# Kernel optimization log

Measured on AMD Instinct MI355X. Metric: run time of the kernel, lower is better.

The kernel has to match this reference:

```python
import jax, jax.numpy as jnp
import numpy as np

DIM = 256
HEADS = 8
HEAD_DIM = DIM // HEADS
SCALE = HEAD_DIM ** -0.5
EPS_LN = 1e-5
EPS_NORM = 1e-12


def setup_inputs() -> dict:
    key = jax.random.key(0)
    ks = jax.random.split(key, 12)
    B, C, H, W = 8, DIM, 32, 32
    s = 0.02
    return {
        "x": jax.random.normal(ks[0], (B, C, H, W), jnp.float32),
        "dw_w": jax.random.normal(ks[1], (C, 1, 3, 3), jnp.float32) * s,
        "dw_b": jnp.zeros((C,), jnp.float32),
        "qkv_w": jax.random.normal(ks[2], (3 * C, C), jnp.float32) * s,
        "c1_w": jax.random.normal(ks[3], (C, C), jnp.float32) * s,
        "c1_b": jnp.zeros((C,), jnp.float32),
        "ln1_g": jnp.ones((C,), jnp.float32),
        "ln1_b": jnp.zeros((C,), jnp.float32),
        "c2_w": jax.random.normal(ks[4], (C, C), jnp.float32) * s,
        "c2_b": jnp.zeros((C,), jnp.float32),
        "ln2_g": jnp.ones((C,), jnp.float32),
        "ln2_b": jnp.zeros((C,), jnp.float32),
    }


def _l2norm(t):
    n = jnp.sqrt(jnp.sum(t * t, axis=-1, keepdims=True))
    return t / jnp.maximum(n, EPS_NORM)


def _layernorm_c(x_nchw, g, b):
    # LayerNorm over channel dim of an NCHW tensor (torch does permute->LN->permute)
    mu = jnp.mean(x_nchw, axis=1, keepdims=True)
    var = jnp.mean((x_nchw - mu) ** 2, axis=1, keepdims=True)
    xn = (x_nchw - mu) * jax.lax.rsqrt(var + EPS_LN)
    return xn * g[None, :, None, None] + b[None, :, None, None]


def _gelu(x):
    return jax.nn.gelu(x, approximate=False)


def reference(x, dw_w, dw_b, qkv_w, c1_w, c1_b, ln1_g, ln1_b, c2_w, c2_b, ln2_g, ln2_b):
    B, C, H, W = x.shape
    identity = x
    # depthwise 3x3 conv
    y = jax.lax.conv_general_dilated(
        x, dw_w, window_strides=(1, 1), padding="SAME",
        dimension_numbers=("NCHW", "OIHW", "NCHW"), feature_group_count=C)
    y = y + dw_b[None, :, None, None]
    # tokens [B, N, C]
    t = y.reshape(B, C, H * W).transpose(0, 2, 1)
    qkv = jnp.einsum("bnc,oc->bno", t, qkv_w)  # [B,N,3C]
    qkv = qkv.reshape(B, H * W, 3, HEADS, HEAD_DIM).transpose(2, 0, 3, 1, 4)
    q, k, v = qkv[0], qkv[1], qkv[2]  # [B,h,N,d]
    q = _l2norm(q)
    k = _l2norm(k)
    attn = jnp.einsum("bhnd,bhmd->bhnm", q, k) * SCALE
    attn = jax.nn.softmax(attn, axis=-1)
    o = jnp.einsum("bhnm,bhmd->bhnd", attn, v)  # [B,h,N,d]
    o = o.transpose(0, 2, 1, 3).reshape(B, H * W, C)
    y = o.transpose(0, 2, 1).reshape(B, C, H, W)
    # conv-MLP branch (1x1 convs as channel GEMMs)
    y = jnp.einsum("bchw,oc->bohw", y, c1_w) + c1_b[None, :, None, None]
    y = _gelu(_layernorm_c(y, ln1_g, ln1_b))
    y = jnp.einsum("bchw,oc->bohw", y, c2_w) + c2_b[None, :, None, None]
    y = _gelu(_layernorm_c(y, ln2_g, ln2_b))
    return identity + y
```

## Files before the change

### kernel.cpp

```cpp
#include <hip/hip_runtime.h>
#include <math.h>

#define DIMC 256
#define NTOK 1024
#define QKVN 768
#define HDIM 32

typedef __attribute__((ext_vector_type(8))) short bf16x8;
typedef __attribute__((ext_vector_type(4))) float f32x4;
typedef __attribute__((ext_vector_type(4))) unsigned short us4;

__device__ __forceinline__ unsigned short f2bf(float f) {
  unsigned u = __float_as_uint(f);
  u += 0x7FFF + ((u >> 16) & 1);
  return (unsigned short)(u >> 16);
}

__device__ __forceinline__ float gelu_f(float y) {
  return 0.5f * y * (1.f + erff(y * 0.70710678118654752f));
}

__global__ void dwconv_k(const float* __restrict__ x, const float* __restrict__ w,
                         const float* __restrict__ b, float* __restrict__ y) {
  int bc = blockIdx.x;
  int c = bc & (DIMC - 1);
  float wr[9];
#pragma unroll
  for (int i = 0; i < 9; i++) wr[i] = w[c * 9 + i];
  float bb = b[c];
  const float* xp = x + (size_t)bc * NTOK;
  float* yp = y + (size_t)bc * NTOK;
  for (int p = threadIdx.x; p < NTOK; p += 256) {
    int hh = p >> 5, ww = p & 31;
    float acc = bb;
#pragma unroll
    for (int dh = 0; dh < 3; dh++) {
      int h2 = hh + dh - 1;
      if ((unsigned)h2 < 32u) {
#pragma unroll
        for (int dw = 0; dw < 3; dw++) {
          int w2 = ww + dw - 1;
          if ((unsigned)w2 < 32u) acc += xp[h2 * 32 + w2] * wr[dh * 3 + dw];
        }
      }
    }
    yp[p] = acc;
  }
}

__global__ void cvt_w_k(const float* __restrict__ w0, const float* __restrict__ w1,
                        const float* __restrict__ w2, unsigned short* __restrict__ Wb) {
  int i = (blockIdx.x * 256 + threadIdx.x) * 4;
  const float* src;
  int off;
  if (i < 196608) { src = w0; off = i; }
  else if (i < 262144) { src = w1; off = i - 196608; }
  else { src = w2; off = i - 262144; }
  float4 v = *(const float4*)(src + off);
  us4 o = {f2bf(v.x), f2bf(v.y), f2bf(v.z), f2bf(v.w)};
  *(us4*)(Wb + i) = o;
}

__global__ void t2b_k(const float* __restrict__ y2, unsigned short* __restrict__ A0) {
  __shared__ float tile[32][33];
  int b = blockIdx.z, c0 = blockIdx.y << 5, s0 = blockIdx.x << 5;
  int t = threadIdx.x;
  int j = t & 31, i0 = t >> 5;
#pragma unroll
  for (int i = i0; i < 32; i += 8)
    tile[i][j] = y2[(size_t)(b * 256 + c0 + i) * 1024 + s0 + j];
  __syncthreads();
#pragma unroll
  for (int i2 = i0; i2 < 32; i2 += 8)
    A0[(size_t)(b * 1024 + s0 + i2) * 256 + c0 + j] = f2bf(tile[j][i2]);
}

template <bool BIAS>
__global__ __launch_bounds__(256) void mgemm_k(const unsigned short* __restrict__ A,
                                               const unsigned short* __restrict__ W,
                                               const float* __restrict__ bias,
                                               float* __restrict__ C, int N) {
  __shared__ __align__(16) unsigned short As[128 * 40];
  __shared__ __align__(16) unsigned short Bs[64 * 40];
  const int t = threadIdx.x;
  const int m0 = blockIdx.y * 128;
  const int n0 = blockIdx.x * 64;
  const int wid = t >> 6, lane = t & 63;
  const int lg = lane >> 4, lr = lane & 15;
  const int wm0 = (wid >> 1) * 64, wn0 = (wid & 1) * 32;

  f32x4 acc[4][2] = {};
  for (int k0 = 0; k0 < 256; k0 += 32) {
    __syncthreads();
    {
#pragma unroll
      for (int u = 0; u < 2; u++) {
        int f = t + u * 256;
        int r = f >> 2, c = f & 3;
        bf16x8 v = *(const bf16x8*)(A + (size_t)(m0 + r) * 256 + k0 + c * 8);
        *(bf16x8*)&As[r * 40 + c * 8] = v;
      }
      int o = t >> 2, c = t & 3;
      bf16x8 v = *(const bf16x8*)(W + (size_t)(n0 + o) * 256 + k0 + c * 8);
      *(bf16x8*)&Bs[o * 40 + c * 8] = v;
    }
    __syncthreads();
    bf16x8 af[4], bfr[2];
#pragma unroll
    for (int mt = 0; mt < 4; mt++)
      af[mt] = *(const bf16x8*)&As[(wm0 + mt * 16 + lr) * 40 + lg * 8];
#pragma unroll
    for (int nt = 0; nt < 2; nt++)
      bfr[nt] = *(const bf16x8*)&Bs[(wn0 + nt * 16 + lr) * 40 + lg * 8];
#pragma unroll
    for (int mt = 0; mt < 4; mt++)
#pragma unroll
      for (int nt = 0; nt < 2; nt++)
        acc[mt][nt] = __builtin_amdgcn_mfma_f32_16x16x32_bf16(af[mt], bfr[nt], acc[mt][nt], 0, 0, 0);
  }
  float bv[2];
#pragma unroll
  for (int nt = 0; nt < 2; nt++)
    bv[nt] = BIAS ? bias[n0 + wn0 + nt * 16 + lr] : 0.f;
#pragma unroll
  for (int mt = 0; mt < 4; mt++)
#pragma unroll
    for (int nt = 0; nt < 2; nt++)
#pragma unroll
      for (int r = 0; r < 4; r++) {
        int row = m0 + wm0 + mt * 16 + lg * 4 + r;
        int col = n0 + wn0 + nt * 16 + lr;
        C[(size_t)row * N + col] = acc[mt][nt][r] + bv[nt];
      }
}

__global__ void cvt_qkv_k(const float* __restrict__ qkv,
                          unsigned short* __restrict__ Qb,
                          unsigned short* __restrict__ Kb) {
  int n = blockIdx.x;
  int t = threadIdx.x;
  int b = n >> 10, nr = n & 1023;
  int sec = t >> 6, lane = t & 63;
  const float* p = qkv + (size_t)n * QKVN + sec * 256 + lane * 4;
  float4 v = *(const float4*)p;
  float s = v.x * v.x + v.y * v.y + v.z * v.z + v.w * v.w;
  s += __shfl_xor(s, 1, 64); s += __shfl_xor(s, 2, 64); s += __shfl_xor(s, 4, 64);
  float inv = 1.f / fmaxf(sqrtf(s), 1e-12f);
  if (sec == 0) inv *= 0.17677669529663687f;
  int h = lane >> 3, d4 = (lane & 7) << 2;
  unsigned short* dst = (sec == 0 ? Qb : Kb) + ((size_t)((b * 8 + h) * 1024 + nr)) * 32 + d4;
  us4 o = {f2bf(v.x * inv), f2bf(v.y * inv), f2bf(v.z * inv), f2bf(v.w * inv)};
  *(us4*)dst = o;
}

#define VPAD 66
__global__ __launch_bounds__(256) void vT_k(const float* __restrict__ qkv,
                                            unsigned short* __restrict__ Vt) {
  __shared__ unsigned short Vl[32 * VPAD];
  const int tt = blockIdx.x, bh = blockIdx.y;
  const int b = bh >> 3, h = bh & 7;
  const int n0 = tt * 64;
  const int t = threadIdx.x;
  {
    int nl = t >> 2, d8 = (t & 3) * 8;
    const float* p = qkv + (size_t)(b * 1024 + n0 + nl) * QKVN + 512 + h * 32 + d8;
    float4 a = *(const float4*)p;
    float4 c = *(const float4*)(p + 4);
    float vv[8] = {a.x, a.y, a.z, a.w, c.x, c.y, c.z, c.w};
#pragma unroll
    for (int i = 0; i < 8; i++) Vl[(d8 + i) * VPAD + nl] = f2bf(vv[i]);
  }
  __syncthreads();
  {
    int d = t >> 3, seg = t & 7;
    us4 lo = *(const us4*)&Vl[d * VPAD + seg * 8];
    us4 hi = *(const us4*)&Vl[d * VPAD + seg * 8 + 4];
    unsigned short* dst = Vt + ((size_t)(bh * 32 + d) << 10) + n0 + seg * 8;
    *(us4*)dst = lo;
    *(us4*)(dst + 4) = hi;
  }
}

#define PSTR 36

__global__ __launch_bounds__(64) void attn_mfma_k(const unsigned short* __restrict__ Qb,
                                                  const unsigned short* __restrict__ Kb,
                                                  const unsigned short* __restrict__ Vt,
                                                  unsigned short* __restrict__ obuf) {
  __shared__ __align__(16) unsigned short Pl[32 * PSTR];
  const int bh = blockIdx.y;
  const int q0 = blockIdx.x * 32;
  const int lane = threadIdx.x;
  const int lg = lane >> 4, lr = lane & 15;
  const size_t base = (size_t)bh * NTOK;
  const unsigned short* vb = Vt + ((size_t)bh * 32 << 10);

  bf16x8 qf[2];
#pragma unroll
  for (int qt = 0; qt < 2; qt++)
    qf[qt] = *(const bf16x8*)(Qb + (base + q0 + qt * 16 + lr) * 32 + lg * 8);

  f32x4 o[2][2] = {};
  float lpart[2][4] = {};

  for (int step = 0; step < 32; step++) {
    const int kv0 = step * 32;
    bf16x8 kf[2];
#pragma unroll
    for (int ct = 0; ct < 2; ct++)
      kf[ct] = *(const bf16x8*)(Kb + (base + kv0 + ct * 16 + lr) * 32 + lg * 8);
#pragma unroll
    for (int qt = 0; qt < 2; qt++) {
#pragma unroll
      for (int ct = 0; ct < 2; ct++) {
        f32x4 c = {};
        c = __builtin_amdgcn_mfma_f32_16x16x32_bf16(qf[qt], kf[ct], c, 0, 0, 0);
#pragma unroll
        for (int r = 0; r < 4; r++) {
          float p = __expf(c[r]);
          lpart[qt][r] += p;
          Pl[(qt * 16 + lg * 4 + r) * PSTR + ct * 16 + lr] = f2bf(p);
        }
      }
    }
#pragma unroll
    for (int qt = 0; qt < 2; qt++) {
      us4 plo = *(const us4*)&Pl[(qt * 16 + lr) * PSTR + lg * 8];
      us4 phi = *(const us4*)&Pl[(qt * 16 + lr) * PSTR + lg * 8 + 4];
      bf16x8 pf = {(short)plo[0], (short)plo[1], (short)plo[2], (short)plo[3],
                   (short)phi[0], (short)phi[1], (short)phi[2], (short)phi[3]};
#pragma unroll
      for (int dt = 0; dt < 2; dt++) {
        bf16x8 vf = *(const bf16x8*)(vb + ((size_t)(dt * 16 + lr) << 10) + kv0 + lg * 8);
        o[qt][dt] = __builtin_amdgcn_mfma_f32_16x16x32_bf16(pf, vf, o[qt][dt], 0, 0, 0);
      }
    }
  }
#pragma unroll
  for (int qt = 0; qt < 2; qt++) {
#pragma unroll
    for (int r = 0; r < 4; r++) {
      float l = lpart[qt][r];
      l += __shfl_xor(l, 1, 64); l += __shfl_xor(l, 2, 64);
      l += __shfl_xor(l, 4, 64); l += __shfl_xor(l, 8, 64);
      lpart[qt][r] = 1.f / l;
    }
  }
  const int b = bh >> 3, h = bh & 7;
#pragma unroll
  for (int qt = 0; qt < 2; qt++)
#pragma unroll
    for (int dt = 0; dt < 2; dt++)
#pragma unroll
      for (int r = 0; r < 4; r++) {
        int q = q0 + qt * 16 + lg * 4 + r;
        int c = h * 32 + dt * 16 + lr;
        obuf[((size_t)(b * NTOK + q)) * DIMC + c] = f2bf(o[qt][dt][r] * lpart[qt][r]);
      }
}

template <bool OBF>
__global__ void ln_gelu_k(const float* __restrict__ in, const float* __restrict__ g,
                          const float* __restrict__ bb, void* __restrict__ outv) {
  int t = threadIdx.x;
  int lane = t & 63;
  int r = blockIdx.x * 4 + (t >> 6);
  const float* p = in + ((size_t)r << 8) + (lane << 2);
  float4 v = *(const float4*)p;
  float s1 = v.x + v.y + v.z + v.w;
  float s2 = v.x * v.x + v.y * v.y + v.z * v.z + v.w * v.w;
#pragma unroll
  for (int m = 1; m < 64; m <<= 1) {
    s1 += __shfl_xor(s1, m, 64);
    s2 += __shfl_xor(s2, m, 64);
  }
  float mu = s1 * (1.f / 256.f);
  float var = s2 * (1.f / 256.f) - mu * mu;
  float rstd = rsqrtf(var + 1e-5f);
  float4 gv = *(const float4*)(g + (lane << 2));
  float4 bv = *(const float4*)(bb + (lane << 2));
  float4 ov;
  ov.x = gelu_f((v.x - mu) * rstd * gv.x + bv.x);
  ov.y = gelu_f((v.y - mu) * rstd * gv.y + bv.y);
  ov.z = gelu_f((v.z - mu) * rstd * gv.z + bv.z);
  ov.w = gelu_f((v.w - mu) * rstd * gv.w + bv.w);
  if (OBF) {
    us4 ob = {f2bf(ov.x), f2bf(ov.y), f2bf(ov.z), f2bf(ov.w)};
    *(us4*)((unsigned short*)outv + ((size_t)r << 8) + (lane << 2)) = ob;
  } else {
    *(float4*)((float*)outv + ((size_t)r << 8) + (lane << 2)) = ov;
  }
}

__global__ void trans_add_k(const float* __restrict__ m2, const float* __restrict__ x,
                            float* __restrict__ out) {
  __shared__ float tile[32][33];
  int b = blockIdx.z, c0 = blockIdx.y << 5, s0 = blockIdx.x << 5;
  int t = threadIdx.x;
  int j = t & 31, i0 = t >> 5;
#pragma unroll
  for (int i = i0; i < 32; i += 8)
    tile[i][j] = m2[(size_t)(b * 1024 + s0 + i) * 256 + c0 + j];
  __syncthreads();
#pragma unroll
  for (int i2 = i0; i2 < 32; i2 += 8) {
    size_t idx = ((size_t)(b * 256 + c0 + i2) << 10) + s0 + j;
    out[idx] = x[idx] + tile[j][i2];
  }
}

extern "C" void kernel_launch(void* const* d_in, const int* in_sizes, int n_in,
                              void* d_out, int out_size, void* d_ws, size_t ws_size,
                              hipStream_t stream) {
  const float* x     = (const float*)d_in[0];
  const float* dw_w  = (const float*)d_in[1];
  const float* dw_b  = (const float*)d_in[2];
  const float* qkv_w = (const float*)d_in[3];
  const float* c1_w  = (const float*)d_in[4];
  const float* c1_b  = (const float*)d_in[5];
  const float* ln1_g = (const float*)d_in[6];
  const float* ln1_b = (const float*)d_in[7];
  const float* c2_w  = (const float*)d_in[8];
  const float* c2_b  = (const float*)d_in[9];
  const float* ln2_g = (const float*)d_in[10];
  const float* ln2_b = (const float*)d_in[11];
  float* out = (float*)d_out;

  float* ws = (float*)d_ws;
  const size_t MF = (size_t)1 << 20;
  float* y2   = ws;
  unsigned short* A0 = (unsigned short*)(ws + 2 * MF);
  unsigned short* Wb = (unsigned short*)(ws + 3 * MF);
  float* qkv  = ws + 4 * MF;
  unsigned short* Qb = (unsigned short*)(ws + 10 * MF);
  unsigned short* Kb = (unsigned short*)(ws + 11 * MF);
  unsigned short* Vtb = (unsigned short*)(ws + 12 * MF);
  unsigned short* obuf = (unsigned short*)ws;
  unsigned short* m1 = (unsigned short*)(ws + 1 * MF);
  float* buf1 = ws + 4 * MF;
  float* buf2 = ws + 6 * MF;
  float* m2b  = ws + 8 * MF;
  (void)in_sizes; (void)n_in; (void)out_size; (void)ws_size;

  dwconv_k<<<2048, 256, 0, stream>>>(x, dw_w, dw_b, y2);
  cvt_w_k<<<320, 256, 0, stream>>>(qkv_w, c1_w, c2_w, Wb);
  t2b_k<<<dim3(32, 8, 8), 256, 0, stream>>>(y2, A0);
  mgemm_k<false><<<dim3(12, 64), 256, 0, stream>>>(A0, Wb, nullptr, qkv, 768);
  cvt_qkv_k<<<8192, 128, 0, stream>>>(qkv, Qb, Kb);
  vT_k<<<dim3(16, 64), 256, 0, stream>>>(qkv, Vtb);
  attn_mfma_k<<<dim3(32, 64), 64, 0, stream>>>(Qb, Kb, Vtb, obuf);
  mgemm_k<true><<<dim3(4, 64), 256, 0, stream>>>(obuf, Wb + 196608, c1_b, buf1, 256);
  ln_gelu_k<true><<<2048, 256, 0, stream>>>(buf1, ln1_g, ln1_b, m1);
  mgemm_k<true><<<dim3(4, 64), 256, 0, stream>>>(m1, Wb + 262144, c2_b, buf2, 256);
  ln_gelu_k<false><<<2048, 256, 0, stream>>>(buf2, ln2_g, ln2_b, m2b);
  trans_add_k<<<dim3(32, 8, 8), 256, 0, stream>>>(m2b, x, out);
}
```

Before: 178.3 us.

## Fuse dwconv with transpose/cast, QK-norm with V transpose, LN2 with residual transpose

Merges the depthwise conv, weight conversion and token-major bf16 transpose into one kernel, so the fp32 conv output no longer makes a round trip through global memory. The Q/K normalisation is folded into the V-transpose kernel, and the second LayerNorm+GELU is fused with the NCHW transpose and residual add through a shared-memory tile. Together these drop three launches and several intermediate buffers. In exchange, the fused LN/transpose kernel runs only 256 blocks with a large shared tile, and the conv kernel reloads halo rows for each block.

```diff
diff --git a/kernel.cpp b/kernel.cpp
--- a/kernel.cpp
+++ b/kernel.cpp
@@ -20,59 +20,64 @@
   return 0.5f * y * (1.f + erff(y * 0.70710678118654752f));
 }
 
-__global__ void dwconv_k(const float* __restrict__ x, const float* __restrict__ w,
-                         const float* __restrict__ b, float* __restrict__ y) {
-  int bc = blockIdx.x;
-  int c = bc & (DIMC - 1);
-  float wr[9];
-#pragma unroll
-  for (int i = 0; i < 9; i++) wr[i] = w[c * 9 + i];
-  float bb = b[c];
-  const float* xp = x + (size_t)bc * NTOK;
-  float* yp = y + (size_t)bc * NTOK;
-  for (int p = threadIdx.x; p < NTOK; p += 256) {
-    int hh = p >> 5, ww = p & 31;
-    float acc = bb;
+__global__ __launch_bounds__(256) void dwt_k(const float* __restrict__ x,
+                                             const float* __restrict__ w,
+                                             const float* __restrict__ b,
+                                             unsigned short* __restrict__ A0,
+                                             const float* __restrict__ w0,
+                                             const float* __restrict__ w1,
+                                             const float* __restrict__ w2,
+                                             unsigned short* __restrict__ Wb) {
+  int blk = blockIdx.x;
+  int t = threadIdx.x;
+  if (blk >= 2048) {
+    int i = ((blk - 2048) * 256 + t) * 4;
+    const float* src;
+    int off;
+    if (i < 196608) { src = w0; off = i; }
+    else if (i < 262144) { src = w1; off = i - 196608; }
+    else { src = w2; off = i - 262144; }
+    float4 v = *(const float4*)(src + off);
+    us4 o = {f2bf(v.x), f2bf(v.y), f2bf(v.z), f2bf(v.w)};
+    *(us4*)(Wb + i) = o;
+    return;
+  }
+  __shared__ float xs[32][3][33];
+  __shared__ float ws9[32][9];
+  __shared__ float bs[32];
+  const int b_ = blk >> 8, h = (blk >> 3) & 31, c0 = (blk & 7) << 5;
+  {
+    int cl = t >> 3, seg = (t & 7) << 2;
+    const float* xp = x + ((size_t)(b_ * 256 + c0 + cl) << 10);
 #pragma unroll
     for (int dh = 0; dh < 3; dh++) {
-      int h2 = hh + dh - 1;
-      if ((unsigned)h2 < 32u) {
-#pragma unroll
-        for (int dw = 0; dw < 3; dw++) {
-          int w2 = ww + dw - 1;
-          if ((unsigned)w2 < 32u) acc += xp[h2 * 32 + w2] * wr[dh * 3 + dw];
-        }
-      }
-    }
-    yp[p] = acc;
-  }
-}
-
-__global__ void cvt_w_k(const float* __restrict__ w0, const float* __restrict__ w1,
-                        const float* __restrict__ w2, unsigned short* __restrict__ Wb) {
-  int i = (blockIdx.x * 256 + threadIdx.x) * 4;
-  const float* src;
-  int off;
-  if (i < 196608) { src = w0; off = i; }
-  else if (i < 262144) { src = w1; off = i - 196608; }
-  else { src = w2; off = i - 262144; }
-  float4 v = *(const float4*)(src + off);
-  us4 o = {f2bf(v.x), f2bf(v.y), f2bf(v.z), f2bf(v.w)};
-  *(us4*)(Wb + i) = o;
-}
-
-__global__ void t2b_k(const float* __restrict__ y2, unsigned short* __restrict__ A0) {
-  __shared__ float tile[32][33];
-  int b = blockIdx.z, c0 = blockIdx.y << 5, s0 = blockIdx.x << 5;
-  int t = threadIdx.x;
-  int j = t & 31, i0 = t >> 5;
-#pragma unroll
-  for (int i = i0; i < 32; i += 8)
-    tile[i][j] = y2[(size_t)(b * 256 + c0 + i) * 1024 + s0 + j];
+      int h2 = h + dh - 1;
+      float4 v = {0.f, 0.f, 0.f, 0.f};
+      if ((unsigned)h2 < 32u) v = *(const float4*)(xp + h2 * 32 + seg);
+      xs[cl][dh][seg + 0] = v.x; xs[cl][dh][seg + 1] = v.y;
+      xs[cl][dh][seg + 2] = v.z; xs[cl][dh][seg + 3] = v.w;
+    }
+  }
+  for (int i = t; i < 288; i += 256) ws9[i / 9][i % 9] = w[(c0 + i / 9) * 9 + i % 9];
+  if (t < 32) bs[t] = b[c0 + t];
   __syncthreads();
-#pragma unroll
-  for (int i2 = i0; i2 < 32; i2 += 8)
-    A0[(size_t)(b * 1024 + s0 + i2) * 256 + c0 + j] = f2bf(tile[j][i2]);
+  const int wp = t >> 3, cq = (t & 7) << 2;
+  us4 o;
+#pragma unroll
+  for (int j = 0; j < 4; j++) {
+    int c = cq + j;
+    float acc = bs[c];
+#pragma unroll
+    for (int dh = 0; dh < 3; dh++) {
+#pragma unroll
+      for (int dw = 0; dw < 3; dw++) {
+        int w2 = wp + dw - 1;
+        if ((unsigned)w2 < 32u) acc += xs[c][dh][w2] * ws9[c][dh * 3 + dw];
+      }
+    }
+    o[j] = f2bf(acc);
+  }
+  *(us4*)(A0 + (((size_t)(b_ * 1024 + h * 32 + wp)) << 8) + c0 + cq) = o;
 }
 
 template <bool BIAS>
@@ -134,33 +139,39 @@
       }
 }
 
-__global__ void cvt_qkv_k(const float* __restrict__ qkv,
-                          unsigned short* __restrict__ Qb,
-                          unsigned short* __restrict__ Kb) {
-  int n = blockIdx.x;
-  int t = threadIdx.x;
-  int b = n >> 10, nr = n & 1023;
-  int sec = t >> 6, lane = t & 63;
-  const float* p = qkv + (size_t)n * QKVN + sec * 256 + lane * 4;
-  float4 v = *(const float4*)p;
-  float s = v.x * v.x + v.y * v.y + v.z * v.z + v.w * v.w;
-  s += __shfl_xor(s, 1, 64); s += __shfl_xor(s, 2, 64); s += __shfl_xor(s, 4, 64);
-  float inv = 1.f / fmaxf(sqrtf(s), 1e-12f);
-  if (sec == 0) inv *= 0.17677669529663687f;
-  int h = lane >> 3, d4 = (lane & 7) << 2;
-  unsigned short* dst = (sec == 0 ? Qb : Kb) + ((size_t)((b * 8 + h) * 1024 + nr)) * 32 + d4;
-  us4 o = {f2bf(v.x * inv), f2bf(v.y * inv), f2bf(v.z * inv), f2bf(v.w * inv)};
-  *(us4*)dst = o;
-}
-
 #define VPAD 66
-__global__ __launch_bounds__(256) void vT_k(const float* __restrict__ qkv,
-                                            unsigned short* __restrict__ Vt) {
+__global__ __launch_bounds__(256) void qkvprep_k(const float* __restrict__ qkv,
+                                                 unsigned short* __restrict__ Qb,
+                                                 unsigned short* __restrict__ Kb,
+                                                 unsigned short* __restrict__ Vt) {
   __shared__ unsigned short Vl[32 * VPAD];
   const int tt = blockIdx.x, bh = blockIdx.y;
   const int b = bh >> 3, h = bh & 7;
   const int n0 = tt * 64;
   const int t = threadIdx.x;
+  {
+    int pair = t >> 7, idx = t & 127;
+    int nl = idx >> 1, e0 = (idx & 1) << 4;
+    const float* p = qkv + (size_t)(b * 1024 + n0 + nl) * QKVN + pair * 256 + h * 32 + e0;
+    float4 v0 = *(const float4*)(p + 0);
+    float4 v1 = *(const float4*)(p + 4);
+    float4 v2 = *(const float4*)(p + 8);
+    float4 v3 = *(const float4*)(p + 12);
+    float s = v0.x * v0.x + v0.y * v0.y + v0.z * v0.z + v0.w * v0.w
+            + v1.x * v1.x + v1.y * v1.y + v1.z * v1.z + v1.w * v1.w
+            + v2.x * v2.x + v2.y * v2.y + v2.z * v2.z + v2.w * v2.w
+            + v3.x * v3.x + v3.y * v3.y + v3.z * v3.z + v3.w * v3.w;
+    s += __shfl_xor(s, 1, 64);
+    float inv = 1.f / fmaxf(sqrtf(s), 1e-12f);
+    if (pair == 0) inv *= 0.17677669529663687f;
+    unsigned short* dst = (pair ? Kb : Qb) + ((size_t)(bh * 1024 + n0 + nl)) * 32 + e0;
+    us4 o0 = {f2bf(v0.x * inv), f2bf(v0.y * inv), f2bf(v0.z * inv), f2bf(v0.w * inv)};
+    us4 o1 = {f2bf(v1.x * inv), f2bf(v1.y * inv), f2bf(v1.z * inv), f2bf(v1.w * inv)};
+    us4 o2 = {f2bf(v2.x * inv), f2bf(v2.y * inv), f2bf(v2.z * inv), f2bf(v2.w * inv)};
+    us4 o3 = {f2bf(v3.x * inv), f2bf(v3.y * inv), f2bf(v3.z * inv), f2bf(v3.w * inv)};
+    *(us4*)(dst + 0) = o0; *(us4*)(dst + 4) = o1;
+    *(us4*)(dst + 8) = o2; *(us4*)(dst + 12) = o3;
+  }
   {
     int nl = t >> 2, d8 = (t & 3) * 8;
     const float* p = qkv + (size_t)(b * 1024 + n0 + nl) * QKVN + 512 + h * 32 + d8;
@@ -259,9 +270,8 @@
       }
 }
 
-template <bool OBF>
 __global__ void ln_gelu_k(const float* __restrict__ in, const float* __restrict__ g,
-                          const float* __restrict__ bb, void* __restrict__ outv) {
+                          const float* __restrict__ bb, unsigned short* __restrict__ out) {
   int t = threadIdx.x;
   int lane = t & 63;
   int r = blockIdx.x * 4 + (t >> 6);
@@ -279,33 +289,51 @@
   float rstd = rsqrtf(var + 1e-5f);
   float4 gv = *(const float4*)(g + (lane << 2));
   float4 bv = *(const float4*)(bb + (lane << 2));
-  float4 ov;
-  ov.x = gelu_f((v.x - mu) * rstd * gv.x + bv.x);
-  ov.y = gelu_f((v.y - mu) * rstd * gv.y + bv.y);
-  ov.z = gelu_f((v.z - mu) * rstd * gv.z + bv.z);
-  ov.w = gelu_f((v.w - mu) * rstd * gv.w + bv.w);
-  if (OBF) {
-    us4 ob = {f2bf(ov.x), f2bf(ov.y), f2bf(ov.z), f2bf(ov.w)};
-    *(us4*)((unsigned short*)outv + ((size_t)r << 8) + (lane << 2)) = ob;
-  } else {
-    *(float4*)((float*)outv + ((size_t)r << 8) + (lane << 2)) = ov;
-  }
-}
-
-__global__ void trans_add_k(const float* __restrict__ m2, const float* __restrict__ x,
-                            float* __restrict__ out) {
-  __shared__ float tile[32][33];
-  int b = blockIdx.z, c0 = blockIdx.y << 5, s0 = blockIdx.x << 5;
-  int t = threadIdx.x;
-  int j = t & 31, i0 = t >> 5;
-#pragma unroll
-  for (int i = i0; i < 32; i += 8)
-    tile[i][j] = m2[(size_t)(b * 1024 + s0 + i) * 256 + c0 + j];
+  us4 ob = {f2bf(gelu_f((v.x - mu) * rstd * gv.x + bv.x)),
+            f2bf(gelu_f((v.y - mu) * rstd * gv.y + bv.y)),
+            f2bf(gelu_f((v.z - mu) * rstd * gv.z + bv.z)),
+            f2bf(gelu_f((v.w - mu) * rstd * gv.w + bv.w))};
+  *(us4*)(out + ((size_t)r << 8) + (lane << 2)) = ob;
+}
+
+__global__ __launch_bounds__(256) void ln_trans_k(const float* __restrict__ in,
+                                                  const float* __restrict__ g,
+                                                  const float* __restrict__ bb,
+                                                  const float* __restrict__ x,
+                                                  float* __restrict__ out) {
+  __shared__ float ys[32][257];
+  const int b = blockIdx.y, s0 = blockIdx.x << 5;
+  const int t = threadIdx.x, lane = t & 63, wv = t >> 6;
+  float gv[4], bv[4];
+#pragma unroll
+  for (int e = 0; e < 4; e++) { gv[e] = g[lane + 64 * e]; bv[e] = bb[lane + 64 * e]; }
+  for (int i = 0; i < 8; i++) {
+    int tok = wv * 8 + i;
+    size_t r = (size_t)(b * 1024 + s0 + tok) << 8;
+    float v[4];
+    float s1 = 0.f, s2 = 0.f;
+#pragma unroll
+    for (int e = 0; e < 4; e++) {
+      v[e] = in[r + lane + 64 * e];
+      s1 += v[e]; s2 += v[e] * v[e];
+    }
+#pragma unroll
+    for (int m = 1; m < 64; m <<= 1) {
+      s1 += __shfl_xor(s1, m, 64);
+      s2 += __shfl_xor(s2, m, 64);
+    }
+    float mu = s1 * (1.f / 256.f);
+    float var = s2 * (1.f / 256.f) - mu * mu;
+    float rstd = rsqrtf(var + 1e-5f);
+#pragma unroll
+    for (int e = 0; e < 4; e++)
+      ys[tok][lane + 64 * e] = gelu_f((v[e] - mu) * rstd * gv[e] + bv[e]);
+  }
   __syncthreads();
-#pragma unroll
-  for (int i2 = i0; i2 < 32; i2 += 8) {
-    size_t idx = ((size_t)(b * 256 + c0 + i2) << 10) + s0 + j;
-    out[idx] = x[idx] + tile[j][i2];
+  const int j = t & 31, cr = t >> 5;
+  for (int c = cr; c < 256; c += 8) {
+    size_t idx = ((size_t)(b * 256 + c) << 10) + s0 + j;
+    out[idx] = x[idx] + ys[j][c];
   }
 }
 
@@ -328,30 +356,24 @@
 
   float* ws = (float*)d_ws;
   const size_t MF = (size_t)1 << 20;
-  float* y2   = ws;
-  unsigned short* A0 = (unsigned short*)(ws + 2 * MF);
-  unsigned short* Wb = (unsigned short*)(ws + 3 * MF);
-  float* qkv  = ws + 4 * MF;
-  unsigned short* Qb = (unsigned short*)(ws + 10 * MF);
-  unsigned short* Kb = (unsigned short*)(ws + 11 * MF);
-  unsigned short* Vtb = (unsigned short*)(ws + 12 * MF);
-  unsigned short* obuf = (unsigned short*)ws;
-  unsigned short* m1 = (unsigned short*)(ws + 1 * MF);
-  float* buf1 = ws + 4 * MF;
-  float* buf2 = ws + 6 * MF;
-  float* m2b  = ws + 8 * MF;
+  unsigned short* Wb = (unsigned short*)ws;
+  unsigned short* A0 = (unsigned short*)(ws + MF / 4);
+  float* qkv  = ws + 2 * MF;
+  unsigned short* Qb = (unsigned short*)(ws + 8 * MF);
+  unsigned short* Kb = (unsigned short*)(ws + 9 * MF);
+  unsigned short* Vtb = (unsigned short*)(ws + 10 * MF);
+  unsigned short* obuf = (unsigned short*)(ws + MF / 4);
+  float* buf1 = ws + 2 * MF;
+  unsigned short* m1 = (unsigned short*)(ws + 4 * MF);
+  float* buf2 = ws + 5 * MF;
   (void)in_sizes; (void)n_in; (void)out_size; (void)ws_size;
 
-  dwconv_k<<<2048, 256, 0, stream>>>(x, dw_w, dw_b, y2);
-  cvt_w_k<<<320, 256, 0, stream>>>(qkv_w, c1_w, c2_w, Wb);
-  t2b_k<<<dim3(32, 8, 8), 256, 0, stream>>>(y2, A0);
+  dwt_k<<<2368, 256, 0, stream>>>(x, dw_w, dw_b, A0, qkv_w, c1_w, c2_w, Wb);
   mgemm_k<false><<<dim3(12, 64), 256, 0, stream>>>(A0, Wb, nullptr, qkv, 768);
-  cvt_qkv_k<<<8192, 128, 0, stream>>>(qkv, Qb, Kb);
-  vT_k<<<dim3(16, 64), 256, 0, stream>>>(qkv, Vtb);
+  qkvprep_k<<<dim3(16, 64), 256, 0, stream>>>(qkv, Qb, Kb, Vtb);
   attn_mfma_k<<<dim3(32, 64), 64, 0, stream>>>(Qb, Kb, Vtb, obuf);
   mgemm_k<true><<<dim3(4, 64), 256, 0, stream>>>(obuf, Wb + 196608, c1_b, buf1, 256);
-  ln_gelu_k<true><<<2048, 256, 0, stream>>>(buf1, ln1_g, ln1_b, m1);
+  ln_gelu_k<<<2048, 256, 0, stream>>>(buf1, ln1_g, ln1_b, m1);
   mgemm_k<true><<<dim3(4, 64), 256, 0, stream>>>(m1, Wb + 262144, c2_b, buf2, 256);
-  ln_gelu_k<false><<<2048, 256, 0, stream>>>(buf2, ln2_g, ln2_b, m2b);
-  trans_add_k<<<dim3(32, 8, 8), 256, 0, stream>>>(m2b, x, out);
-}
+  ln_trans_k<<<dim3(32, 8), 256, 0, stream>>>(buf2, ln2_g, ln2_b, x, out);
+}
```

Result: faster. 169.5 us (-4.9%).
